# Optimization experiments

Measured on AMD Instinct MI355X. Metric: run time of the kernel, lower is better.

## Reference

```python
import jax, jax.numpy as jnp
import numpy as np

N, E, G = 8000, 128000, 4
C, NLM, NL = 64, 16, 4
NEL, NB, NH = 10, 8, 64
RMAX = 5.0
PCUT = 5.0
AVG_NEIGH = 16.0
SIGMA = 1.0
LBOX = 6.0
KR = 3
T = 2
LMAP = jnp.array([0, 1, 1, 1, 2, 2, 2, 2, 2, 3, 3, 3, 3, 3, 3, 3])


def _nvec():
    r = np.arange(-KR, KR + 1)
    n = np.stack(np.meshgrid(r, r, r, indexing='ij'), -1).reshape(-1, 3)
    n = n[np.any(n != 0, axis=1)]  # [342,3], k=0 excluded
    return jnp.asarray(n, jnp.float32)


def sph_harm(u):
    # component-normalized real spherical harmonics up to l=3, unit input u [E,3]
    x, y, z = u[:, 0], u[:, 1], u[:, 2]
    one = jnp.ones_like(x)
    c3, c5, c15 = 3.0 ** 0.5, 5.0 ** 0.5, 15.0 ** 0.5
    Y = [one,
         c3 * x, c3 * y, c3 * z,
         c15 * x * y, c15 * y * z, 0.5 * c5 * (3 * z * z - 1.0), c15 * x * z, 0.5 * c15 * (x * x - y * y),
         (35.0 / 8.0) ** 0.5 * y * (3 * x * x - y * y), 105.0 ** 0.5 * x * y * z,
         (21.0 / 8.0) ** 0.5 * y * (5 * z * z - 1.0), 0.5 * 7.0 ** 0.5 * z * (5 * z * z - 3.0),
         (21.0 / 8.0) ** 0.5 * x * (5 * z * z - 1.0), 0.5 * 105.0 ** 0.5 * z * (x * x - y * y),
         (35.0 / 8.0) ** 0.5 * x * (x * x - 3 * y * y)]
    return jnp.stack(Y, -1)  # [E,16]


def radial_basis(r):
    # Bessel basis * polynomial cutoff (MACE RadialEmbeddingBlock)
    u = r / RMAX
    n = jnp.arange(1, NB + 1, dtype=jnp.float32)
    bes = (2.0 / RMAX) ** 0.5 * jnp.sin(n[None, :] * jnp.pi * u[:, None]) / (r[:, None] + 1e-9)
    p = PCUT
    fc = 1.0 - 0.5 * (p + 1) * (p + 2) * u ** p + p * (p + 2) * u ** (p + 1) - 0.5 * p * (p + 1) * u ** (p + 2)
    fc = fc * (u < 1.0)
    return bes * fc[:, None]  # [E,8]


def setup_inputs() -> dict:
    key = jax.random.key(0)
    ks = jax.random.split(key, 24)

    def p(k, shape, fan_in):
        return jax.random.normal(k, shape, jnp.float32) / (fan_in ** 0.5)

    elem = jax.random.randint(ks[0], (N,), 0, NEL)
    inp = {
        'node_attrs': jax.nn.one_hot(elem, NEL, dtype=jnp.float32),
        'positions': jax.random.uniform(ks[1], (N, 3), jnp.float32) * LBOX,
        'shifts': jnp.zeros((E, 3), jnp.float32),
        'density_coefficients': jax.random.normal(ks[2], (N, 1), jnp.float32) * 0.1,
        'cell': jnp.tile(jnp.eye(3, dtype=jnp.float32) * LBOX, (G, 1, 1)),
        'rcell': jnp.tile(jnp.eye(3, dtype=jnp.float32) / LBOX, (G, 1, 1)),
        'volume': jnp.full((G,), LBOX ** 3, jnp.float32),
        'edge_index': jax.random.randint(ks[3], (2, E), 0, N),
        'batch': jnp.repeat(jnp.arange(G), N // G),
        'emb_W': p(ks[4], (NEL, C), NEL),
        'q_coef': p(ks[5], (T, C), 1),
        'rad_W1': p(ks[6], (T, NB, NH), NB),
        'rad_W2': p(ks[7], (T, NH, NH), NH),
        'rad_W3': p(ks[8], (T, NH, NH), NH),
        'rad_W4': p(ks[9], (T, NH, C * NL), NH),
        'lin_up': p(ks[10], (T, NL, C, C), C),
        'lin_out': p(ks[11], (T, NL, C, C), C),
        'W_sc': p(ks[12], (T, NEL, C, C), C),
        'Wp': p(ks[13], (T, 3, C, C), C),
        'W_read0': p(ks[14], (C,), C),
        'Wread1_a': p(ks[15], (C, 16), C),
        'Wread1_b': p(ks[16], (16,), 16),
        'Wq_read': p(ks[17], (T, C), C),
        'atomic_E': jax.random.normal(ks[18], (NEL,), jnp.float32),
    }
    return inp


def reference(node_attrs, positions, shifts, density_coefficients, cell, rcell, volume,
              edge_index, batch, emb_W, q_coef, rad_W1, rad_W2, rad_W3, rad_W4,
              lin_up, lin_out, W_sc, Wp, W_read0, Wread1_a, Wread1_b, Wq_read, atomic_E):
    sender, receiver = edge_index[0], edge_index[1]
    vec = positions[receiver] - positions[sender] + shifts
    r = jnp.linalg.norm(vec, axis=-1)
    Y = sph_harm(vec / (r[:, None] + 1e-9))      # [E,16]
    ef = radial_basis(r)                          # [E,8]

    q = density_coefficients                      # [N,1], max_l=0 multipoles
    feats = jnp.zeros((N, C, NLM), jnp.float32).at[:, :, 0].set(node_attrs @ emb_W)
    e0 = jax.ops.segment_sum(node_attrs @ atomic_E, batch, G)
    energies = [e0]

    for t in range(T):
        # charge-coefficient injection (charge_coefs_linears)
        feats = feats.at[:, :, 0].add(q * q_coef[t][None, :])
        # per-l linear up
        h = jnp.einsum('ncl,lcd->ndl', feats, lin_up[t][LMAP])
        # radial MLP -> per-edge, per-channel, per-l tensor-product weights
        w = jax.nn.silu(ef @ rad_W1[t])
        w = jax.nn.silu(w @ rad_W2[t])
        w = jax.nn.silu(w @ rad_W3[t])
        w = (w @ rad_W4[t]).reshape(E, C, NL)[:, :, LMAP]   # [E,C,16]
        # depthwise equivariant TP message: gather -> contract -> modulate
        hj = h[sender]                                       # [E,C,16]
        s_e = jnp.einsum('ecl,el->ec', hj, Y)                # edge invariant
        m = w * (Y[:, None, :] * s_e[:, :, None])            # [E,C,16]
        A = jax.ops.segment_sum(m, receiver, N) / AVG_NEIGH  # scatter-reduce
        A = jnp.einsum('ncl,lcd->ndl', A, lin_out[t][LMAP])
        # element-dependent residual (self-connection)
        wn = jnp.einsum('nk,kcd->ncd', node_attrs, W_sc[t])
        sc = jnp.einsum('ncd,ncl->ndl', wn, feats)
        # product block: correlation-3 symmetric-contraction surrogate
        s1 = jnp.sum(A * A, axis=2)                           # [N,C]
        out = (jnp.einsum('ncl,cd->ndl', A, Wp[t, 0])
               + jnp.einsum('ncl,cd->ndl', A * s1[:, :, None], Wp[t, 1])
               + jnp.einsum('ncl,cd->ndl', A * (s1 * s1)[:, :, None], Wp[t, 2]))
        feats = out + sc
        # readout
        if t == T - 1:
            node_e = jax.nn.silu(feats[:, :, 0] @ Wread1_a) @ Wread1_b
        else:
            node_e = feats[:, :, 0] @ W_read0
        node_e = node_e + q[:, 0] * (feats[:, :, 0] @ Wq_read[t])
        energies.append(jax.ops.segment_sum(node_e, batch, G))

    # k-space (Ewald-like) electrostatics with Gaussian-smeared charges
    nv = _nvec()                                              # [K,3]
    kvec = 2.0 * jnp.pi * jnp.einsum('kj,gji->gki', nv, rcell)  # [G,K,3]
    k2 = jnp.sum(kvec * kvec, -1)                             # [G,K]
    phase = jnp.einsum('ni,nki->nk', positions, kvec[batch])  # [N,K]
    Sr = jax.ops.segment_sum(q * jnp.cos(phase), batch, G)
    Si = jax.ops.segment_sum(q * jnp.sin(phase), batch, G)
    filt = jnp.exp(-0.5 * SIGMA * SIGMA * k2) / k2
    Ees = (2.0 * jnp.pi / volume) * jnp.sum(filt * (Sr * Sr + Si * Si), axis=1)

    total_energy = jnp.sum(jnp.stack(energies, -1), -1) + Ees
    total_charge = jax.ops.segment_sum(q[:, 0], batch, G)
    dipole = jax.ops.segment_sum(q * positions, batch, G)
    return total_energy, total_charge, dipole
```

## Files before the change

### kernel.cpp

```cpp
#include <hip/hip_runtime.h>
#include <hip/hip_bf16.h>

constexpr int N    = 8000;
constexpr int E    = 128000;
constexpr int G    = 4;
constexpr int NEL  = 10;
constexpr int NGR  = N / G;
constexpr int NC   = N * 64;
constexpr int NK   = 342;
constexpr float RMAX = 5.0f;
constexpr int XS = 68;
constexpr int HS = 72;
constexpr int WT_T = 25088;

typedef __bf16 bf16x8 __attribute__((ext_vector_type(8)));
typedef float  f32x4v __attribute__((ext_vector_type(4)));
typedef unsigned short u16x8 __attribute__((ext_vector_type(8)));

__device__ __forceinline__ int lmap_rt(int l) { return (l >= 1) + (l >= 4) + (l >= 9); }
__device__ __forceinline__ float silu(float x) { return x / (1.f + __expf(-x)); }
__device__ __forceinline__ float bf2f(unsigned short u) { return __uint_as_float(((unsigned)u) << 16); }
__device__ __forceinline__ unsigned short f2bf(float f) {
    __hip_bfloat16 h = __float2bfloat16(f);
    return *(unsigned short*)&h;
}

__device__ __forceinline__ void gemm64(const float* X, const float* W,
                                       int tr, int tc, float4 acc[4])
{
    #pragma unroll 2
    for (int k0 = 0; k0 < 64; k0 += 4) {
        float4 xq[4];
        #pragma unroll
        for (int j = 0; j < 4; ++j) xq[j] = *(const float4*)&X[((tr << 2) + j) * XS + k0];
        #pragma unroll
        for (int i = 0; i < 4; ++i) {
            const float4 w = *(const float4*)&W[((k0 + i) << 6) + (tc << 2)];
            #pragma unroll
            for (int j = 0; j < 4; ++j) {
                const float x = ((const float*)&xq[j])[i];
                acc[j].x += x * w.x; acc[j].y += x * w.y; acc[j].z += x * w.z; acc[j].w += x * w.w;
            }
        }
    }
}

__device__ __forceinline__ void mfma_stage(const unsigned short* hsrc, const unsigned short* wt,
                                           int m0, int lane, f32x4v acc[4], bool k8only)
{
    const int quad = lane >> 4;
    const int idx  = lane & 15;
    bf16x8 bz;
    #pragma unroll
    for (int i = 0; i < 8; ++i) bz[i] = (__bf16)0.f;
    bf16x8 a0 = bz, a1 = bz;
    const int mrow = m0 + idx;
    if (k8only) {
        if (quad == 0) a0 = *(const bf16x8*)&hsrc[mrow * HS];
    } else {
        a0 = *(const bf16x8*)&hsrc[mrow * HS + (quad << 3)];
        a1 = *(const bf16x8*)&hsrc[mrow * HS + 32 + (quad << 3)];
    }
    #pragma unroll
    for (int c4 = 0; c4 < 4; ++c4) {
        const int nrow = (c4 << 4) + idx;
        if (k8only) {
            bf16x8 b0 = bz;
            if (quad == 0) b0 = *(const bf16x8*)&wt[nrow * HS];
            acc[c4] = __builtin_amdgcn_mfma_f32_16x16x32_bf16(a0, b0, acc[c4], 0, 0, 0);
        } else {
            const bf16x8 b0 = *(const bf16x8*)&wt[nrow * HS + (quad << 3)];
            const bf16x8 b1 = *(const bf16x8*)&wt[nrow * HS + 32 + (quad << 3)];
            acc[c4] = __builtin_amdgcn_mfma_f32_16x16x32_bf16(a0, b0, acc[c4], 0, 0, 0);
            acc[c4] = __builtin_amdgcn_mfma_f32_16x16x32_bf16(a1, b1, acc[c4], 0, 0, 0);
        }
    }
}

__global__ __launch_bounds__(256) void k_init(const float* __restrict__ na,
    const float* __restrict__ q, const float* __restrict__ pos,
    const int* __restrict__ batch, const float* __restrict__ aE,
    int* __restrict__ elem, float* __restrict__ acc)
{
    __shared__ float s[G * 5];
    if (threadIdx.x < G * 5) s[threadIdx.x] = 0.f;
    __syncthreads();
    const int n = blockIdx.x * 256 + threadIdx.x;
    if (n < N) {
        int el = 0; float best = na[n * NEL];
        #pragma unroll
        for (int j = 1; j < NEL; ++j) { float v = na[n * NEL + j]; if (v > best) { best = v; el = j; } }
        elem[n] = el;
        const int g = batch[n];
        const float qn = q[n];
        atomicAdd(&s[g * 5 + 0], aE[el]);
        atomicAdd(&s[g * 5 + 1], qn);
        atomicAdd(&s[g * 5 + 2], qn * pos[n * 3 + 0]);
        atomicAdd(&s[g * 5 + 3], qn * pos[n * 3 + 1]);
        atomicAdd(&s[g * 5 + 4], qn * pos[n * 3 + 2]);
    }
    __syncthreads();
    if (threadIdx.x < G * 5) atomicAdd(&acc[threadIdx.x], s[threadIdx.x]);
}

__global__ __launch_bounds__(256) void k_feat0(const int* __restrict__ elem,
    const float* __restrict__ embW, float* __restrict__ F)
{
    const int i = blockIdx.x * 256 + threadIdx.x;
    if (i < NC) F[i] = embW[elem[i >> 6] * 64 + (i & 63)];
}

__global__ __launch_bounds__(256) void k_pre(const float* __restrict__ q,
    const float* __restrict__ qc, float* __restrict__ F)
{
    const int i = blockIdx.x * 256 + threadIdx.x;
    if (i < NC) F[i] += q[i >> 6] * qc[i & 63];
}

__global__ __launch_bounds__(256) void k_hist(const int* __restrict__ elem, int* __restrict__ counts)
{
    const int n = blockIdx.x * 256 + threadIdx.x;
    if (n < N) atomicAdd(&counts[elem[n]], 1);
}
__global__ void k_offs(const int* __restrict__ counts, int* __restrict__ offs)
{
    if (threadIdx.x == 0 && blockIdx.x == 0) {
        int o = 0;
        for (int j = 0; j < NEL; ++j) { offs[j] = o; o += (counts[j] + 63) & ~63; }
        offs[NEL] = o;
    }
}
__global__ __launch_bounds__(256) void k_scatter(const int* __restrict__ elem,
    const int* __restrict__ offs, int* __restrict__ cursor, int* __restrict__ perm)
{
    const int n = blockIdx.x * 256 + threadIdx.x;
    if (n < N) {
        const int el = elem[n];
        const int p = atomicAdd(&cursor[el], 1);
        perm[offs[el] + p] = n;
    }
}

__global__ __launch_bounds__(256) void k_gcnt(const int* __restrict__ ei, int* __restrict__ cnt)
{
    const int e = blockIdx.x * 256 + threadIdx.x;
    if (e < E) atomicAdd(&cnt[ei[E + e]], 1);
}
__global__ __launch_bounds__(1024) void k_goff(const int* __restrict__ cnt, int* __restrict__ roff)
{
    __shared__ int part[1024];
    const int t = threadIdx.x;
    const int base = t * 8;
    int loc[8];
    int s = 0;
    #pragma unroll
    for (int i = 0; i < 8; ++i) { loc[i] = s; s += (base + i < N) ? cnt[base + i] : 0; }
    part[t] = s;
    __syncthreads();
    for (int d = 1; d < 1024; d <<= 1) {
        const int v = (t >= d) ? part[t - d] : 0;
        __syncthreads();
        part[t] += v;
        __syncthreads();
    }
    const int excl = (t == 0) ? 0 : part[t - 1];
    #pragma unroll
    for (int i = 0; i < 8; ++i) if (base + i < N) roff[base + i] = excl + loc[i];
    if (t == 0) roff[N] = E;
}
__global__ __launch_bounds__(256) void k_gscat(const int* __restrict__ ei,
    const int* __restrict__ roff, int* __restrict__ cur, int* __restrict__ elist)
{
    const int e = blockIdx.x * 256 + threadIdx.x;
    if (e < E) {
        const int rv = ei[E + e];
        const int p = atomicAdd(&cur[rv], 1);
        elist[roff[rv] + p] = e;
    }
}

__global__ __launch_bounds__(256) void k_geom(const float* __restrict__ pos,
    const float* __restrict__ shifts, const int* __restrict__ ei,
    const int* __restrict__ elist, float4* __restrict__ geomv, int* __restrict__ spck)
{
    const int j = blockIdx.x * 256 + threadIdx.x;
    if (j >= E) return;
    const int e = elist[j];
    const int s = ei[e], rv = ei[E + e];
    const float dx = pos[rv * 3 + 0] - pos[s * 3 + 0] + shifts[e * 3 + 0];
    const float dy = pos[rv * 3 + 1] - pos[s * 3 + 1] + shifts[e * 3 + 1];
    const float dz = pos[rv * 3 + 2] - pos[s * 3 + 2] + shifts[e * 3 + 2];
    const float r = sqrtf(dx * dx + dy * dy + dz * dz);
    const float inv = 1.f / (r + 1e-9f);
    float4 g;
    g.x = dx * inv; g.y = dy * inv; g.z = dz * inv; g.w = r;
    geomv[j] = g;
    spck[j] = s;
}

__global__ __launch_bounds__(256) void k_wprep(const float* __restrict__ rW1,
    const float* __restrict__ rW2, const float* __restrict__ rW3,
    const float* __restrict__ rW4, unsigned short* __restrict__ WT)
{
    const int idx = blockIdx.x * 256 + threadIdx.x;
    if (idx >= 2 * WT_T) return;
    const int t = idx / WT_T;
    const int r = idx % WT_T;
    float v;
    if (r < 512) {
        const int n = r >> 3, k = r & 7;
        v = rW1[t * 512 + k * 64 + n];
    } else if (r < 4608) {
        const int i = r - 512, n = i >> 6, k = i & 63;
        v = rW2[t * 4096 + k * 64 + n];
    } else if (r < 8704) {
        const int i = r - 4608, n = i >> 6, k = i & 63;
        v = rW3[t * 4096 + k * 64 + n];
    } else {
        const int i = r - 8704, n = i >> 6, k = i & 63;
        v = rW4[t * 16384 + k * 256 + n];
    }
    WT[idx] = f2bf(v);
}

__global__ __launch_bounds__(256) void k_wprep2(const float* __restrict__ Wp,
    unsigned short* __restrict__ WpT)
{
    const int idx = blockIdx.x * 256 + threadIdx.x;
    if (idx >= 24576) return;
    const int tp = idx / 4096;
    const int i  = idx % 4096;
    const int d = i >> 6, c = i & 63;
    WpT[idx] = f2bf(Wp[(size_t)tp * 4096 + c * 64 + d]);
}

__global__ __launch_bounds__(256) void k_lgemm_hb(const float* __restrict__ X,
    const float* __restrict__ Wb, unsigned short* __restrict__ Hb)
{
    __shared__ float Ws[4096];
    __shared__ float Xs[64 * XS];
    const int l  = blockIdx.y;
    const int nb = blockIdx.x << 6;
    const float* W = Wb + lmap_rt(l) * 4096;
    for (int i = threadIdx.x; i < 4096; i += 256) Ws[i] = W[i];
    const float* Xp = X + (size_t)l * NC + (size_t)nb * 64;
    for (int i = threadIdx.x; i < 4096; i += 256) Xs[(i >> 6) * XS + (i & 63)] = Xp[i];
    __syncthreads();
    const int tc = threadIdx.x & 15;
    const int tr = threadIdx.x >> 4;
    float4 acc[4];
    #pragma unroll
    for (int j = 0; j < 4; ++j) acc[j] = make_float4(0.f, 0.f, 0.f, 0.f);
    gemm64(Xs, Ws, tr, tc, acc);
    #pragma unroll
    for (int j = 0; j < 4; ++j) {
        const int n = nb + (tr << 2) + j;
        ushort4 o;
        o.x = f2bf(acc[j].x); o.y = f2bf(acc[j].y); o.z = f2bf(acc[j].z); o.w = f2bf(acc[j].w);
        *(ushort4*)&Hb[(size_t)n * 1024 + (l << 6) + (tc << 2)] = o;
    }
}

__global__ __launch_bounds__(256) void k_lgemm(const float* __restrict__ X,
    const float* __restrict__ Wb, float* __restrict__ Out)
{
    __shared__ float Ws[4096];
    __shared__ float Xs[64 * XS];
    const int l  = blockIdx.y;
    const int nb = blockIdx.x << 6;
    const float* W = Wb + lmap_rt(l) * 4096;
    for (int i = threadIdx.x; i < 4096; i += 256) Ws[i] = W[i];
    const float* Xp = X + (size_t)l * NC + (size_t)nb * 64;
    for (int i = threadIdx.x; i < 4096; i += 256) Xs[(i >> 6) * XS + (i & 63)] = Xp[i];
    __syncthreads();
    const int tc = threadIdx.x & 15;
    const int tr = threadIdx.x >> 4;
    float4 acc[4];
    #pragma unroll
    for (int j = 0; j < 4; ++j) acc[j] = make_float4(0.f, 0.f, 0.f, 0.f);
    gemm64(Xs, Ws, tr, tc, acc);
    float* Op = Out + (size_t)l * NC + (size_t)nb * 64;
    #pragma unroll
    for (int j = 0; j < 4; ++j)
        *(float4*)&Op[(((tr << 2) + j) << 6) + (tc << 2)] = acc[j];
}

__global__ __launch_bounds__(256) void k_sc(const float* __restrict__ F,
    const float* __restrict__ Wsc, const int* __restrict__ perm,
    const int* __restrict__ elem, float* __restrict__ Out)
{
    __shared__ float Ws[4096];
    __shared__ float Xs[64 * XS];
    __shared__ int rows[64];
    const int l  = blockIdx.y;
    const int tb = blockIdx.x << 6;
    if (threadIdx.x < 64) rows[threadIdx.x] = perm[tb + threadIdx.x];
    __syncthreads();
    if (rows[0] < 0) return;
    const float* W = Wsc + elem[rows[0]] * 4096;
    for (int i = threadIdx.x; i < 4096; i += 256) Ws[i] = W[i];
    for (int i = threadIdx.x; i < 4096; i += 256) {
        const int rr = i >> 6, cc = i & 63;
        const int n = rows[rr];
        Xs[rr * XS + cc] = (n >= 0) ? F[(size_t)l * NC + (size_t)n * 64 + cc] : 0.f;
    }
    __syncthreads();
    const int tc = threadIdx.x & 15;
    const int tr = threadIdx.x >> 4;
    float4 acc[4];
    #pragma unroll
    for (int j = 0; j < 4; ++j) acc[j] = make_float4(0.f, 0.f, 0.f, 0.f);
    gemm64(Xs, Ws, tr, tc, acc);
    #pragma unroll
    for (int j = 0; j < 4; ++j) {
        const int n = rows[(tr << 2) + j];
        if (n >= 0) *(float4*)&Out[(size_t)l * NC + (size_t)n * 64 + (tc << 2)] = acc[j];
    }
}

__global__ __launch_bounds__(256) void k_wgemm(const float4* __restrict__ geomv,
    const unsigned short* __restrict__ WT, unsigned short* __restrict__ wout)
{
    __shared__ unsigned short hbf[64 * HS];
    __shared__ unsigned short wtb[2][64 * HS];
    __shared__ unsigned short outS[64 * HS];
    const int t = threadIdx.x;
    const int lane = t & 63;
    const int wid  = t >> 6;
    const int m0   = wid << 4;
    const int quad = lane >> 4;
    const int idx  = lane & 15;
    const int j0 = blockIdx.x << 6;
    if (t < 64) {
        const float r = geomv[j0 + t].w;
        const float u  = r * 0.2f;
        const float u2 = u * u, u5 = u2 * u2 * u;
        const float fc = 1.f - 21.f * u5 + 35.f * u5 * u - 15.f * u5 * u2;
        float pref = 0.63245553f * fc / (r + 1e-9f);
        if (u >= 1.f) pref = 0.f;
        const float piu = 3.14159265358979f * u;
        #pragma unroll
        for (int b = 0; b < 8; ++b) hbf[t * HS + b] = f2bf(__sinf((float)(b + 1) * piu) * pref);
    }
    {
        const int n = t >> 2, k = (t & 3) << 1;
        wtb[0][n * HS + k]     = WT[n * 8 + k];
        wtb[0][n * HS + k + 1] = WT[n * 8 + k + 1];
    }
    const int prow = t >> 2, pkb = (t & 3) << 4;
    u16x8 pf0, pf1;
    pf0 = *(const u16x8*)&WT[512 + prow * 64 + pkb];
    pf1 = *(const u16x8*)&WT[512 + prow * 64 + pkb + 8];
    __syncthreads();
    f32x4v acc[4];
    #pragma unroll
    for (int c = 0; c < 4; ++c) { acc[c][0] = 0.f; acc[c][1] = 0.f; acc[c][2] = 0.f; acc[c][3] = 0.f; }
    mfma_stage(hbf, wtb[0], m0, lane, acc, true);
    __syncthreads();
    #pragma unroll
    for (int c4 = 0; c4 < 4; ++c4)
        #pragma unroll
        for (int r = 0; r < 4; ++r)
            hbf[(m0 + (quad << 2) + r) * HS + (c4 << 4) + idx] = f2bf(silu(acc[c4][r]));
    *(u16x8*)&wtb[1][prow * HS + pkb]     = pf0;
    *(u16x8*)&wtb[1][prow * HS + pkb + 8] = pf1;
    pf0 = *(const u16x8*)&WT[4608 + prow * 64 + pkb];
    pf1 = *(const u16x8*)&WT[4608 + prow * 64 + pkb + 8];
    __syncthreads();
    #pragma unroll
    for (int c = 0; c < 4; ++c) { acc[c][0] = 0.f; acc[c][1] = 0.f; acc[c][2] = 0.f; acc[c][3] = 0.f; }
    mfma_stage(hbf, wtb[1], m0, lane, acc, false);
    __syncthreads();
    #pragma unroll
    for (int c4 = 0; c4 < 4; ++c4)
        #pragma unroll
        for (int r = 0; r < 4; ++r)
            hbf[(m0 + (quad << 2) + r) * HS + (c4 << 4) + idx] = f2bf(silu(acc[c4][r]));
    *(u16x8*)&wtb[0][prow * HS + pkb]     = pf0;
    *(u16x8*)&wtb[0][prow * HS + pkb + 8] = pf1;
    pf0 = *(const u16x8*)&WT[8704 + prow * 64 + pkb];
    pf1 = *(const u16x8*)&WT[8704 + prow * 64 + pkb + 8];
    __syncthreads();
    #pragma unroll
    for (int c = 0; c < 4; ++c) { acc[c][0] = 0.f; acc[c][1] = 0.f; acc[c][2] = 0.f; acc[c][3] = 0.f; }
    mfma_stage(hbf, wtb[0], m0, lane, acc, false);
    __syncthreads();
    #pragma unroll
    for (int c4 = 0; c4 < 4; ++c4)
        #pragma unroll
        for (int r = 0; r < 4; ++r)
            hbf[(m0 + (quad << 2) + r) * HS + (c4 << 4) + idx] = f2bf(silu(acc[c4][r]));
    *(u16x8*)&wtb[1][prow * HS + pkb]     = pf0;
    *(u16x8*)&wtb[1][prow * HS + pkb + 8] = pf1;
    pf0 = *(const u16x8*)&WT[8704 + 4096 + prow * 64 + pkb];
    pf1 = *(const u16x8*)&WT[8704 + 4096 + prow * 64 + pkb + 8];
    __syncthreads();
    int cur = 1;
    for (int c = 0; c < 4; ++c) {
        #pragma unroll
        for (int cc = 0; cc < 4; ++cc) { acc[cc][0] = 0.f; acc[cc][1] = 0.f; acc[cc][2] = 0.f; acc[cc][3] = 0.f; }
        mfma_stage(hbf, wtb[cur], m0, lane, acc, false);
        __syncthreads();
        #pragma unroll
        for (int c4 = 0; c4 < 4; ++c4)
            #pragma unroll
            for (int r = 0; r < 4; ++r)
                outS[(m0 + (quad << 2) + r) * HS + (c4 << 4) + idx] = f2bf(acc[c4][r]);
        if (c < 3) {
            *(u16x8*)&wtb[1 - cur][prow * HS + pkb]     = pf0;
            *(u16x8*)&wtb[1 - cur][prow * HS + pkb + 8] = pf1;
            if (c < 2) {
                pf0 = *(const u16x8*)&WT[8704 + (c + 2) * 4096 + prow * 64 + pkb];
                pf1 = *(const u16x8*)&WT[8704 + (c + 2) * 4096 + prow * 64 + pkb + 8];
            }
        }
        __syncthreads();
        *(u16x8*)&wout[(size_t)(j0 + prow) * 256 + (c << 6) + pkb]     = *(const u16x8*)&outS[prow * HS + pkb];
        *(u16x8*)&wout[(size_t)(j0 + prow) * 256 + (c << 6) + pkb + 8] = *(const u16x8*)&outS[prow * HS + pkb + 8];
        cur ^= 1;
    }
}

__global__ __launch_bounds__(256) void k_agg(const float4* __restrict__ geomv,
    const int* __restrict__ spck,
    const unsigned short* __restrict__ Hb, const unsigned short* __restrict__ wb,
    const int* __restrict__ roff, float* __restrict__ A)
{
    const int lane = threadIdx.x & 63;
    const int n = (blockIdx.x << 2) + (threadIdx.x >> 6);
    const int ja = roff[n], jb2 = roff[n + 1];
    float acc[16];
    #pragma unroll
    for (int l = 0; l < 16; ++l) acc[l] = 0.f;
    constexpr int LM[16] = {0,1,1,1,2,2,2,2,2,3,3,3,3,3,3,3};
    float4 g0, g1;
    ushort4 w0, w1;
    int s1_ = 0;
    unsigned short hv0[16];
    if (ja < jb2) {
        g0 = geomv[ja];
        const int s0 = spck[ja];
        w0 = *(const ushort4*)&wb[(size_t)ja * 256 + (lane << 2)];
        #pragma unroll
        for (int l = 0; l < 16; ++l) hv0[l] = Hb[(size_t)s0 * 1024 + (l << 6) + lane];
    }
    if (ja + 1 < jb2) {
        g1 = geomv[ja + 1];
        s1_ = spck[ja + 1];
        w1 = *(const ushort4*)&wb[(size_t)(ja + 1) * 256 + (lane << 2)];
    }
    for (int j = ja; j < jb2; ++j) {
        const float4 gc = g0;
        const ushort4 wc = w0;
        float hc[16];
        #pragma unroll
        for (int l = 0; l < 16; ++l) hc[l] = bf2f(hv0[l]);
        if (j + 1 < jb2) {
            g0 = g1; w0 = w1;
            const int sN = s1_;
            #pragma unroll
            for (int l = 0; l < 16; ++l) hv0[l] = Hb[(size_t)sN * 1024 + (l << 6) + lane];
            if (j + 2 < jb2) {
                g1 = geomv[j + 2];
                s1_ = spck[j + 2];
                w1 = *(const ushort4*)&wb[(size_t)(j + 2) * 256 + (lane << 2)];
            }
        }
        if (gc.w >= RMAX) continue;
        const float x = gc.x, y = gc.y, z = gc.z;
        const float xx = x * x, yy = y * y, zz = z * z;
        float Y[16];
        Y[0] = 1.f;
        Y[1] = 1.7320508f * x;  Y[2] = 1.7320508f * y;  Y[3] = 1.7320508f * z;
        Y[4] = 3.8729833f * x * y;  Y[5] = 3.8729833f * y * z;
        Y[6] = 0.5f * 2.2360680f * (3.f * zz - 1.f);
        Y[7] = 3.8729833f * x * z;  Y[8] = 0.5f * 3.8729833f * (xx - yy);
        Y[9]  = 2.0916500f * y * (3.f * xx - yy);
        Y[10] = 10.2469508f * x * y * z;
        Y[11] = 1.6201852f * y * (5.f * zz - 1.f);
        Y[12] = 0.5f * 2.6457513f * z * (5.f * zz - 3.f);
        Y[13] = 1.6201852f * x * (5.f * zz - 1.f);
        Y[14] = 0.5f * 10.2469508f * z * (xx - yy);
        Y[15] = 2.0916500f * x * (xx - 3.f * yy);
        float se = 0.f;
        #pragma unroll
        for (int l = 0; l < 16; ++l) se += hc[l] * Y[l];
        se *= 0.0625f;
        const float wl[4] = { bf2f(wc.x) * se, bf2f(wc.y) * se, bf2f(wc.z) * se, bf2f(wc.w) * se };
        #pragma unroll
        for (int l = 0; l < 16; ++l) acc[l] += wl[LM[l]] * Y[l];
    }
    float* Ap = A + (size_t)n * 64 + lane;
    #pragma unroll
    for (int l = 0; l < 16; ++l) Ap[(size_t)l * NC] = acc[l];
}

__global__ __launch_bounds__(256) void k_s1(const float* __restrict__ H, float* __restrict__ s1)
{
    const int i = blockIdx.x * 256 + threadIdx.x;
    if (i < NC) {
        float s = 0.f;
        #pragma unroll
        for (int l = 0; l < 16; ++l) { const float a = H[(size_t)l * NC + i]; s += a * a; }
        s1[i] = s;
    }
}

__global__ __launch_bounds__(256) void k_out(const float* __restrict__ Ap,
    const float* __restrict__ s1, const unsigned short* __restrict__ WpT,
    const float* __restrict__ sc, float* __restrict__ F)
{
    __shared__ unsigned short Xb[64 * HS];
    __shared__ unsigned short Wt[64 * HS];
    const int l  = blockIdx.y;
    const int nb = blockIdx.x << 6;
    const int t  = threadIdx.x;
    const int lane = t & 63;
    const int m0   = (t >> 6) << 4;
    const int quad = lane >> 4;
    const int idx  = lane & 15;
    const int prow = t >> 2, pkb = (t & 3) << 4;
    const float* Xp = Ap + (size_t)l * NC + (size_t)nb * 64;
    float av[16], sv[16];
    #pragma unroll
    for (int k = 0; k < 16; ++k) {
        const int i = t + (k << 8);
        av[k] = Xp[i];
        sv[k] = s1[nb * 64 + i];
    }
    f32x4v acc[4];
    #pragma unroll
    for (int c = 0; c < 4; ++c) { acc[c][0] = 0.f; acc[c][1] = 0.f; acc[c][2] = 0.f; acc[c][3] = 0.f; }
    for (int p = 0; p < 3; ++p) {
        #pragma unroll
        for (int k = 0; k < 16; ++k) {
            const int i = t + (k << 8);
            Xb[(i >> 6) * HS + (i & 63)] = f2bf(av[k]);
            av[k] *= sv[k];
        }
        *(u16x8*)&Wt[prow * HS + pkb]     = *(const u16x8*)&WpT[p * 4096 + prow * 64 + pkb];
        *(u16x8*)&Wt[prow * HS + pkb + 8] = *(const u16x8*)&WpT[p * 4096 + prow * 64 + pkb + 8];
        __syncthreads();
        mfma_stage(Xb, Wt, m0, lane, acc, false);
        __syncthreads();
    }
    #pragma unroll
    for (int c4 = 0; c4 < 4; ++c4) {
        #pragma unroll
        for (int r = 0; r < 4; ++r) {
            const int row = m0 + (quad << 2) + r;
            const int col = (c4 << 4) + idx;
            const size_t id = (size_t)l * NC + (size_t)(nb + row) * 64 + col;
            F[id] = acc[c4][r] + sc[id];
        }
    }
}

__global__ __launch_bounds__(256) void k_read(const float* __restrict__ F,
    const float* __restrict__ q, const int* __restrict__ batch,
    const float* __restrict__ Wr0, const float* __restrict__ Wa,
    const float* __restrict__ Wb, const float* __restrict__ Wq,
    float* __restrict__ acc, int last)
{
    __shared__ float sred[G];
    if (threadIdx.x < G) sred[threadIdx.x] = 0.f;
    __syncthreads();
    const int n = blockIdx.x * 256 + threadIdx.x;
    if (n < N) {
        float a16[16];
        #pragma unroll
        for (int j = 0; j < 16; ++j) a16[j] = 0.f;
        float ar = 0.f, aq = 0.f;
        const float* f = F + (size_t)n * 64;
        for (int c = 0; c < 64; ++c) {
            const float fv = f[c];
            aq += fv * Wq[c];
            if (last) {
                #pragma unroll
                for (int j = 0; j < 16; ++j) a16[j] += fv * Wa[c * 16 + j];
            } else ar += fv * Wr0[c];
        }
        float en;
        if (last) {
            en = 0.f;
            #pragma unroll
            for (int j = 0; j < 16; ++j) en += silu(a16[j]) * Wb[j];
        } else en = ar;
        en += q[n] * aq;
        atomicAdd(&sred[batch[n]], en);
    }
    __syncthreads();
    if (threadIdx.x < G) atomicAdd(&acc[threadIdx.x * 5], sred[threadIdx.x]);
}

__global__ __launch_bounds__(256) void k_kvec(const float* __restrict__ rcell,
    float* __restrict__ kvec, float* __restrict__ k2)
{
    const int idx = blockIdx.x * 256 + threadIdx.x;
    if (idx >= G * NK) return;
    const int g = idx / NK, k = idx % NK;
    const int kk = k + (k >= 171 ? 1 : 0);
    const int a = kk / 49 - 3, b = (kk / 7) % 7 - 3, c = kk % 7 - 3;
    const float* rc = rcell + g * 9;
    float s = 0.f;
    #pragma unroll
    for (int i = 0; i < 3; ++i) {
        const float kv = 6.283185307f * ((float)a * rc[0 + i] + (float)b * rc[3 + i] + (float)c * rc[6 + i]);
        kvec[idx * 3 + i] = kv;
        s += kv * kv;
    }
    k2[idx] = s;
}

__global__ __launch_bounds__(256) void k_phase(const float* __restrict__ pos,
    const float* __restrict__ q, const float* __restrict__ kvec,
    float* __restrict__ Sr, float* __restrict__ Si)
{
    __shared__ float kvs[38 * 3];
    __shared__ float srs[38], sis[38];
    const int g = blockIdx.z, kc = blockIdx.x, ncb = blockIdx.y;
    const int kbase = kc * 38;
    if (threadIdx.x < 38 * 3) kvs[threadIdx.x] = kvec[((size_t)g * NK + kbase) * 3 + threadIdx.x];
    if (threadIdx.x < 38) { srs[threadIdx.x] = 0.f; sis[threadIdx.x] = 0.f; }
    __syncthreads();
    const int t = threadIdx.x;
    float px = 0.f, py = 0.f, pz = 0.f, qn = 0.f;
    if (t < 250) {
        const int n = g * NGR + ncb * 250 + t;
        px = pos[n * 3]; py = pos[n * 3 + 1]; pz = pos[n * 3 + 2]; qn = q[n];
    }
    const int lane = t & 63;
    for (int j = 0; j < 38; ++j) {
        const float ph = px * kvs[j * 3] + py * kvs[j * 3 + 1] + pz * kvs[j * 3 + 2];
        float sv, cv;
        __sincosf(ph, &sv, &cv);
        float vr = qn * cv, vi = qn * sv;
        #pragma unroll
        for (int o = 32; o > 0; o >>= 1) { vr += __shfl_down(vr, o, 64); vi += __shfl_down(vi, o, 64); }
        if (lane == 0) { atomicAdd(&srs[j], vr); atomicAdd(&sis[j], vi); }
    }
    __syncthreads();
    if (t < 38) {
        atomicAdd(&Sr[g * NK + kbase + t], srs[t]);
        atomicAdd(&Si[g * NK + kbase + t], sis[t]);
    }
}

__global__ __launch_bounds__(512) void k_final(const float* __restrict__ k2,
    const float* __restrict__ Sr, const float* __restrict__ Si,
    const float* __restrict__ vol, const float* __restrict__ acc,
    float* __restrict__ out)
{
    __shared__ float red[512];
    const int g = blockIdx.x, t = threadIdx.x;
    float v = 0.f;
    if (t < NK) {
        const float kk = k2[g * NK + t];
        const float sr = Sr[g * NK + t], si = Si[g * NK + t];
        v = __expf(-0.5f * kk) * (sr * sr + si * si) / kk;
    }
    red[t] = v;
    __syncthreads();
    for (int s2 = 256; s2 > 0; s2 >>= 1) {
        if (t < s2) red[t] += red[t + s2];
        __syncthreads();
    }
    if (t == 0) {
        const float Ees = 6.283185307f / vol[g] * red[0];
        out[g]     = acc[g * 5 + 0] + Ees;
        out[4 + g] = acc[g * 5 + 1];
        out[8 + g * 3 + 0] = acc[g * 5 + 2];
        out[8 + g * 3 + 1] = acc[g * 5 + 3];
        out[8 + g * 3 + 2] = acc[g * 5 + 4];
    }
}

extern "C" void kernel_launch(void* const* d_in, const int* in_sizes, int n_in,
                              void* d_out, int out_size, void* d_ws, size_t ws_size,
                              hipStream_t stream)
{
    const float* na    = (const float*)d_in[0];
    const float* pos   = (const float*)d_in[1];
    const float* shif  = (const float*)d_in[2];
    const float* q     = (const float*)d_in[3];
    const float* rcell = (const float*)d_in[5];
    const float* vol   = (const float*)d_in[6];
    const int*   ei    = (const int*)d_in[7];
    const int*   batch = (const int*)d_in[8];
    const float* embW  = (const float*)d_in[9];
    const float* qcoef = (const float*)d_in[10];
    const float* rW1   = (const float*)d_in[11];
    const float* rW2   = (const float*)d_in[12];
    const float* rW3   = (const float*)d_in[13];
    const float* rW4   = (const float*)d_in[14];
    const float* lup   = (const float*)d_in[15];
    const float* lout  = (const float*)d_in[16];
    const float* Wsc   = (const float*)d_in[17];
    const float* Wp    = (const float*)d_in[18];
    const float* Wr0   = (const float*)d_in[19];
    const float* Wa    = (const float*)d_in[20];
    const float* Wb    = (const float*)d_in[21];
    const float* Wq    = (const float*)d_in[22];
    const float* aE    = (const float*)d_in[23];
    float* out = (float*)d_out;

    float* wsf  = (float*)d_ws;
    float* F    = wsf;
    float* A    = F + 8192000;
    float* R    = A + 8192000;
    float* H2   = R;
    unsigned short* Hb = (unsigned short*)R;
    unsigned short* wb = (unsigned short*)(R + 4096000);
    float* s1   = R + 20480000;
    float* kvec = s1 + 512000;
    float* k2   = kvec + 4104;
    float* Sr   = k2 + 1368;
    float* Si   = Sr + 1368;
    float* acc  = Si + 1368;
    int*   elem = (int*)(acc + 32);
    int*   perm = elem + 8000;
    int*   counts = perm + 8640;
    int*   cursor = counts + 16;
    int*   offs   = cursor + 16;
    int*   roff   = offs + 16;
    int*   cnt    = roff + 8001;
    int*   cur    = cnt + 8000;
    int*   elist  = cur + 8000;
    unsigned short* WTb = (unsigned short*)(((uintptr_t)(elist + E) + 31) & ~(uintptr_t)31);
    unsigned short* WpT = WTb + 2 * WT_T;
    float4* geomv = (float4*)(WpT + 24576);
    int*    spck  = (int*)(geomv + E);

    hipMemsetAsync(F, 0, 8192000 * sizeof(float), stream);
    hipMemsetAsync(Sr, 0, (1368 * 2 + 32) * sizeof(float), stream);
    hipMemsetAsync(perm, 0xFF, 8640 * sizeof(int), stream);
    hipMemsetAsync(counts, 0, 32 * sizeof(int), stream);
    hipMemsetAsync(cnt, 0, 16000 * sizeof(int), stream);

    k_init<<<32, 256, 0, stream>>>(na, q, pos, batch, aE, elem, acc);
    k_feat0<<<2000, 256, 0, stream>>>(elem, embW, F);
    k_hist<<<32, 256, 0, stream>>>(elem, counts);
    k_offs<<<1, 64, 0, stream>>>(counts, offs);
    k_scatter<<<32, 256, 0, stream>>>(elem, offs, cursor, perm);
    k_gcnt<<<500, 256, 0, stream>>>(ei, cnt);
    k_goff<<<1, 1024, 0, stream>>>(cnt, roff);
    k_gscat<<<500, 256, 0, stream>>>(ei, roff, cur, elist);
    k_geom<<<500, 256, 0, stream>>>(pos, shif, ei, elist, geomv, spck);
    k_wprep<<<196, 256, 0, stream>>>(rW1, rW2, rW3, rW4, WTb);
    k_wprep2<<<96, 256, 0, stream>>>(Wp, WpT);
    k_kvec<<<6, 256, 0, stream>>>(rcell, kvec, k2);
    k_phase<<<dim3(9, 8, G), 256, 0, stream>>>(pos, q, kvec, Sr, Si);

    for (int t = 0; t < 2; ++t) {
        k_pre<<<2000, 256, 0, stream>>>(q, qcoef + t * 64, F);
        k_lgemm_hb<<<dim3(125, 16), 256, 0, stream>>>(F, lup + t * 4 * 4096, Hb);
        k_wgemm<<<2000, 256, 0, stream>>>(geomv, WTb + t * WT_T, wb);
        k_agg<<<2000, 256, 0, stream>>>(geomv, spck, Hb, wb, roff, A);
        k_lgemm<<<dim3(125, 16), 256, 0, stream>>>(A, lout + t * 4 * 4096, H2);
        k_s1<<<2000, 256, 0, stream>>>(H2, s1);
        k_sc<<<dim3(135, 16), 256, 0, stream>>>(F, Wsc + t * NEL * 4096, perm, elem, A);
        k_out<<<dim3(125, 16), 256, 0, stream>>>(H2, s1, WpT + t * 12288, A, F);
        k_read<<<32, 256, 0, stream>>>(F, q, batch, Wr0, Wa, Wb, Wq + t * 64, acc, t == 1);
    }
    k_final<<<G, 512, 0, stream>>>(k2, Sr, Si, vol, acc, out);
}
```

Measured before the change: 649.5 us.

## Move per-l channel GEMMs to bf16 MFMA and deepen agg edge prefetch

The three 64x64 fp32 FMA GEMM kernels (lgemm_hb, lgemm, sc) now convert inputs to bf16 in shared memory and use the existing MFMA stage. Their weights are pre-transposed into bf16 by a new prep kernel. The aggregation kernel's edge loop is restructured with a three-deep clamped prefetch of geometry, weights and source indices. This cuts FMA issue and shared-memory traffic, but lowers GEMM input precision to bf16 and adds a prep launch.

New measurement: 564.4 us. -13.1%, faster.

```diff
diff --git a/kernel.cpp b/kernel.cpp
--- a/kernel.cpp
+++ b/kernel.cpp
@@ -9,7 +9,6 @@
 constexpr int NC   = N * 64;
 constexpr int NK   = 342;
 constexpr float RMAX = 5.0f;
-constexpr int XS = 68;
 constexpr int HS = 72;
 constexpr int WT_T = 25088;
 
@@ -23,26 +22,6 @@
 __device__ __forceinline__ unsigned short f2bf(float f) {
     __hip_bfloat16 h = __float2bfloat16(f);
     return *(unsigned short*)&h;
-}
-
-__device__ __forceinline__ void gemm64(const float* X, const float* W,
-                                       int tr, int tc, float4 acc[4])
-{
-    #pragma unroll 2
-    for (int k0 = 0; k0 < 64; k0 += 4) {
-        float4 xq[4];
-        #pragma unroll
-        for (int j = 0; j < 4; ++j) xq[j] = *(const float4*)&X[((tr << 2) + j) * XS + k0];
-        #pragma unroll
-        for (int i = 0; i < 4; ++i) {
-            const float4 w = *(const float4*)&W[((k0 + i) << 6) + (tc << 2)];
-            #pragma unroll
-            for (int j = 0; j < 4; ++j) {
-                const float x = ((const float*)&xq[j])[i];
-                acc[j].x += x * w.x; acc[j].y += x * w.y; acc[j].z += x * w.z; acc[j].w += x * w.w;
-            }
-        }
-    }
 }
 
 __device__ __forceinline__ void mfma_stage(const unsigned short* hsrc, const unsigned short* wt,
@@ -234,87 +213,142 @@
     WpT[idx] = f2bf(Wp[(size_t)tp * 4096 + c * 64 + d]);
 }
 
+__global__ __launch_bounds__(256) void k_wprep3(const float* __restrict__ lup,
+    const float* __restrict__ lout, const float* __restrict__ Wsc,
+    unsigned short* __restrict__ WlupT, unsigned short* __restrict__ WloutT,
+    unsigned short* __restrict__ WscT)
+{
+    const int idx = blockIdx.x * 256 + threadIdx.x;
+    if (idx < 32768) {
+        const int i = idx & 4095, d = i >> 6, c = i & 63;
+        WlupT[idx] = f2bf(lup[(idx >> 12) * 4096 + c * 64 + d]);
+    } else if (idx < 65536) {
+        const int r = idx - 32768;
+        const int i = r & 4095, d = i >> 6, c = i & 63;
+        WloutT[r] = f2bf(lout[(r >> 12) * 4096 + c * 64 + d]);
+    } else if (idx < 147456) {
+        const int r = idx - 65536;
+        const int i = r & 4095, d = i >> 6, c = i & 63;
+        WscT[r] = f2bf(Wsc[(r >> 12) * 4096 + c * 64 + d]);
+    }
+}
+
 __global__ __launch_bounds__(256) void k_lgemm_hb(const float* __restrict__ X,
-    const float* __restrict__ Wb, unsigned short* __restrict__ Hb)
-{
-    __shared__ float Ws[4096];
-    __shared__ float Xs[64 * XS];
+    const unsigned short* __restrict__ WT, unsigned short* __restrict__ Hb)
+{
+    __shared__ unsigned short Xb[64 * HS];
+    __shared__ unsigned short Wt[64 * HS];
     const int l  = blockIdx.y;
     const int nb = blockIdx.x << 6;
-    const float* W = Wb + lmap_rt(l) * 4096;
-    for (int i = threadIdx.x; i < 4096; i += 256) Ws[i] = W[i];
+    const int t  = threadIdx.x;
+    const int lane = t & 63;
+    const int m0   = (t >> 6) << 4;
+    const int quad = lane >> 4;
+    const int idx  = lane & 15;
+    const int prow = t >> 2, pkb = (t & 3) << 4;
     const float* Xp = X + (size_t)l * NC + (size_t)nb * 64;
-    for (int i = threadIdx.x; i < 4096; i += 256) Xs[(i >> 6) * XS + (i & 63)] = Xp[i];
-    __syncthreads();
-    const int tc = threadIdx.x & 15;
-    const int tr = threadIdx.x >> 4;
-    float4 acc[4];
-    #pragma unroll
-    for (int j = 0; j < 4; ++j) acc[j] = make_float4(0.f, 0.f, 0.f, 0.f);
-    gemm64(Xs, Ws, tr, tc, acc);
-    #pragma unroll
-    for (int j = 0; j < 4; ++j) {
-        const int n = nb + (tr << 2) + j;
-        ushort4 o;
-        o.x = f2bf(acc[j].x); o.y = f2bf(acc[j].y); o.z = f2bf(acc[j].z); o.w = f2bf(acc[j].w);
-        *(ushort4*)&Hb[(size_t)n * 1024 + (l << 6) + (tc << 2)] = o;
+    #pragma unroll
+    for (int k = 0; k < 16; ++k) {
+        const int i = t + (k << 8);
+        Xb[(i >> 6) * HS + (i & 63)] = f2bf(Xp[i]);
+    }
+    const unsigned short* W = WT + lmap_rt(l) * 4096;
+    *(u16x8*)&Wt[prow * HS + pkb]     = *(const u16x8*)&W[prow * 64 + pkb];
+    *(u16x8*)&Wt[prow * HS + pkb + 8] = *(const u16x8*)&W[prow * 64 + pkb + 8];
+    __syncthreads();
+    f32x4v acc[4];
+    #pragma unroll
+    for (int c = 0; c < 4; ++c) { acc[c][0] = 0.f; acc[c][1] = 0.f; acc[c][2] = 0.f; acc[c][3] = 0.f; }
+    mfma_stage(Xb, Wt, m0, lane, acc, false);
+    #pragma unroll
+    for (int c4 = 0; c4 < 4; ++c4) {
+        #pragma unroll
+        for (int r = 0; r < 4; ++r) {
+            const int n = nb + m0 + (quad << 2) + r;
+            const int col = (c4 << 4) + idx;
+            Hb[(size_t)n * 1024 + (l << 6) + col] = f2bf(acc[c4][r]);
+        }
     }
 }
 
 __global__ __launch_bounds__(256) void k_lgemm(const float* __restrict__ X,
-    const float* __restrict__ Wb, float* __restrict__ Out)
-{
-    __shared__ float Ws[4096];
-    __shared__ float Xs[64 * XS];
+    const unsigned short* __restrict__ WT, float* __restrict__ Out)
+{
+    __shared__ unsigned short Xb[64 * HS];
+    __shared__ unsigned short Wt[64 * HS];
     const int l  = blockIdx.y;
     const int nb = blockIdx.x << 6;
-    const float* W = Wb + lmap_rt(l) * 4096;
-    for (int i = threadIdx.x; i < 4096; i += 256) Ws[i] = W[i];
+    const int t  = threadIdx.x;
+    const int lane = t & 63;
+    const int m0   = (t >> 6) << 4;
+    const int quad = lane >> 4;
+    const int idx  = lane & 15;
+    const int prow = t >> 2, pkb = (t & 3) << 4;
     const float* Xp = X + (size_t)l * NC + (size_t)nb * 64;
-    for (int i = threadIdx.x; i < 4096; i += 256) Xs[(i >> 6) * XS + (i & 63)] = Xp[i];
-    __syncthreads();
-    const int tc = threadIdx.x & 15;
-    const int tr = threadIdx.x >> 4;
-    float4 acc[4];
-    #pragma unroll
-    for (int j = 0; j < 4; ++j) acc[j] = make_float4(0.f, 0.f, 0.f, 0.f);
-    gemm64(Xs, Ws, tr, tc, acc);
+    #pragma unroll
+    for (int k = 0; k < 16; ++k) {
+        const int i = t + (k << 8);
+        Xb[(i >> 6) * HS + (i & 63)] = f2bf(Xp[i]);
+    }
+    const unsigned short* W = WT + lmap_rt(l) * 4096;
+    *(u16x8*)&Wt[prow * HS + pkb]     = *(const u16x8*)&W[prow * 64 + pkb];
+    *(u16x8*)&Wt[prow * HS + pkb + 8] = *(const u16x8*)&W[prow * 64 + pkb + 8];
+    __syncthreads();
+    f32x4v acc[4];
+    #pragma unroll
+    for (int c = 0; c < 4; ++c) { acc[c][0] = 0.f; acc[c][1] = 0.f; acc[c][2] = 0.f; acc[c][3] = 0.f; }
+    mfma_stage(Xb, Wt, m0, lane, acc, false);
     float* Op = Out + (size_t)l * NC + (size_t)nb * 64;
     #pragma unroll
-    for (int j = 0; j < 4; ++j)
-        *(float4*)&Op[(((tr << 2) + j) << 6) + (tc << 2)] = acc[j];
+    for (int c4 = 0; c4 < 4; ++c4) {
+        #pragma unroll
+        for (int r = 0; r < 4; ++r) {
+            const int row = m0 + (quad << 2) + r;
+            Op[(row << 6) + (c4 << 4) + idx] = acc[c4][r];
+        }
+    }
 }
 
 __global__ __launch_bounds__(256) void k_sc(const float* __restrict__ F,
-    const float* __restrict__ Wsc, const int* __restrict__ perm,
+    const unsigned short* __restrict__ WscT, const int* __restrict__ perm,
     const int* __restrict__ elem, float* __restrict__ Out)
 {
-    __shared__ float Ws[4096];
-    __shared__ float Xs[64 * XS];
+    __shared__ unsigned short Xb[64 * HS];
+    __shared__ unsigned short Wt[64 * HS];
     __shared__ int rows[64];
     const int l  = blockIdx.y;
     const int tb = blockIdx.x << 6;
-    if (threadIdx.x < 64) rows[threadIdx.x] = perm[tb + threadIdx.x];
+    const int t  = threadIdx.x;
+    if (t < 64) rows[t] = perm[tb + t];
     __syncthreads();
     if (rows[0] < 0) return;
-    const float* W = Wsc + elem[rows[0]] * 4096;
-    for (int i = threadIdx.x; i < 4096; i += 256) Ws[i] = W[i];
-    for (int i = threadIdx.x; i < 4096; i += 256) {
+    const int lane = t & 63;
+    const int m0   = (t >> 6) << 4;
+    const int quad = lane >> 4;
+    const int idx  = lane & 15;
+    const int prow = t >> 2, pkb = (t & 3) << 4;
+    const unsigned short* W = WscT + elem[rows[0]] * 4096;
+    *(u16x8*)&Wt[prow * HS + pkb]     = *(const u16x8*)&W[prow * 64 + pkb];
+    *(u16x8*)&Wt[prow * HS + pkb + 8] = *(const u16x8*)&W[prow * 64 + pkb + 8];
+    #pragma unroll
+    for (int k = 0; k < 16; ++k) {
+        const int i = t + (k << 8);
         const int rr = i >> 6, cc = i & 63;
         const int n = rows[rr];
-        Xs[rr * XS + cc] = (n >= 0) ? F[(size_t)l * NC + (size_t)n * 64 + cc] : 0.f;
-    }
-    __syncthreads();
-    const int tc = threadIdx.x & 15;
-    const int tr = threadIdx.x >> 4;
-    float4 acc[4];
-    #pragma unroll
-    for (int j = 0; j < 4; ++j) acc[j] = make_float4(0.f, 0.f, 0.f, 0.f);
-    gemm64(Xs, Ws, tr, tc, acc);
-    #pragma unroll
-    for (int j = 0; j < 4; ++j) {
-        const int n = rows[(tr << 2) + j];
-        if (n >= 0) *(float4*)&Out[(size_t)l * NC + (size_t)n * 64 + (tc << 2)] = acc[j];
+        Xb[rr * HS + cc] = (n >= 0) ? f2bf(F[(size_t)l * NC + (size_t)n * 64 + cc]) : (unsigned short)0;
+    }
+    __syncthreads();
+    f32x4v acc[4];
+    #pragma unroll
+    for (int c = 0; c < 4; ++c) { acc[c][0] = 0.f; acc[c][1] = 0.f; acc[c][2] = 0.f; acc[c][3] = 0.f; }
+    mfma_stage(Xb, Wt, m0, lane, acc, false);
+    #pragma unroll
+    for (int c4 = 0; c4 < 4; ++c4) {
+        #pragma unroll
+        for (int r = 0; r < 4; ++r) {
+            const int n = rows[m0 + (quad << 2) + r];
+            if (n >= 0) Out[(size_t)l * NC + (size_t)n * 64 + (c4 << 4) + idx] = acc[c4][r];
+        }
     }
 }
 
@@ -429,70 +463,68 @@
     const int lane = threadIdx.x & 63;
     const int n = (blockIdx.x << 2) + (threadIdx.x >> 6);
     const int ja = roff[n], jb2 = roff[n + 1];
-    float acc[16];
-    #pragma unroll
-    for (int l = 0; l < 16; ++l) acc[l] = 0.f;
+    float accv[16];
+    #pragma unroll
+    for (int l = 0; l < 16; ++l) accv[l] = 0.f;
     constexpr int LM[16] = {0,1,1,1,2,2,2,2,2,3,3,3,3,3,3,3};
-    float4 g0, g1;
-    ushort4 w0, w1;
-    int s1_ = 0;
-    unsigned short hv0[16];
     if (ja < jb2) {
-        g0 = geomv[ja];
-        const int s0 = spck[ja];
-        w0 = *(const ushort4*)&wb[(size_t)ja * 256 + (lane << 2)];
-        #pragma unroll
-        for (int l = 0; l < 16; ++l) hv0[l] = Hb[(size_t)s0 * 1024 + (l << 6) + lane];
-    }
-    if (ja + 1 < jb2) {
-        g1 = geomv[ja + 1];
-        s1_ = spck[ja + 1];
-        w1 = *(const ushort4*)&wb[(size_t)(ja + 1) * 256 + (lane << 2)];
-    }
-    for (int j = ja; j < jb2; ++j) {
-        const float4 gc = g0;
-        const ushort4 wc = w0;
-        float hc[16];
-        #pragma unroll
-        for (int l = 0; l < 16; ++l) hc[l] = bf2f(hv0[l]);
-        if (j + 1 < jb2) {
-            g0 = g1; w0 = w1;
-            const int sN = s1_;
+        const int jlast = jb2 - 1;
+        int j1c = ja + 1 < jlast ? ja + 1 : jlast;
+        int j2c = ja + 2 < jlast ? ja + 2 : jlast;
+        float4 g0 = geomv[ja],  g1 = geomv[j1c],  g2 = geomv[j2c];
+        ushort4 w0 = *(const ushort4*)&wb[(size_t)ja * 256 + (lane << 2)];
+        ushort4 w1 = *(const ushort4*)&wb[(size_t)j1c * 256 + (lane << 2)];
+        ushort4 w2 = *(const ushort4*)&wb[(size_t)j2c * 256 + (lane << 2)];
+        int sB = spck[j1c], sC = spck[j2c];
+        unsigned short hv[16];
+        {
+            const int s0 = spck[ja];
             #pragma unroll
-            for (int l = 0; l < 16; ++l) hv0[l] = Hb[(size_t)sN * 1024 + (l << 6) + lane];
-            if (j + 2 < jb2) {
-                g1 = geomv[j + 2];
-                s1_ = spck[j + 2];
-                w1 = *(const ushort4*)&wb[(size_t)(j + 2) * 256 + (lane << 2)];
+            for (int l = 0; l < 16; ++l) hv[l] = Hb[(size_t)s0 * 1024 + (l << 6) + lane];
+        }
+        for (int j = ja; j < jb2; ++j) {
+            const float4 gc = g0;
+            const ushort4 wc = w0;
+            float hc[16];
+            #pragma unroll
+            for (int l = 0; l < 16; ++l) hc[l] = bf2f(hv[l]);
+            g0 = g1; g1 = g2; w0 = w1; w1 = w2;
+            const int sA = sB; sB = sC;
+            #pragma unroll
+            for (int l = 0; l < 16; ++l) hv[l] = Hb[(size_t)sA * 1024 + (l << 6) + lane];
+            const int j3 = j + 3 < jlast ? j + 3 : jlast;
+            g2 = geomv[j3];
+            w2 = *(const ushort4*)&wb[(size_t)j3 * 256 + (lane << 2)];
+            sC = spck[j3];
+            if (gc.w < RMAX) {
+                const float x = gc.x, y = gc.y, z = gc.z;
+                const float xx = x * x, yy = y * y, zz = z * z;
+                float Y[16];
+                Y[0] = 1.f;
+                Y[1] = 1.7320508f * x;  Y[2] = 1.7320508f * y;  Y[3] = 1.7320508f * z;
+                Y[4] = 3.8729833f * x * y;  Y[5] = 3.8729833f * y * z;
+                Y[6] = 0.5f * 2.2360680f * (3.f * zz - 1.f);
+                Y[7] = 3.8729833f * x * z;  Y[8] = 0.5f * 3.8729833f * (xx - yy);
+                Y[9]  = 2.0916500f * y * (3.f * xx - yy);
+                Y[10] = 10.2469508f * x * y * z;
+                Y[11] = 1.6201852f * y * (5.f * zz - 1.f);
+                Y[12] = 0.5f * 2.6457513f * z * (5.f * zz - 3.f);
+                Y[13] = 1.6201852f * x * (5.f * zz - 1.f);
+                Y[14] = 0.5f * 10.2469508f * z * (xx - yy);
+                Y[15] = 2.0916500f * x * (xx - 3.f * yy);
+                float se = 0.f;
+                #pragma unroll
+                for (int l = 0; l < 16; ++l) se += hc[l] * Y[l];
+                se *= 0.0625f;
+                const float wl[4] = { bf2f(wc.x) * se, bf2f(wc.y) * se, bf2f(wc.z) * se, bf2f(wc.w) * se };
+                #pragma unroll
+                for (int l = 0; l < 16; ++l) accv[l] += wl[LM[l]] * Y[l];
             }
         }
-        if (gc.w >= RMAX) continue;
-        const float x = gc.x, y = gc.y, z = gc.z;
-        const float xx = x * x, yy = y * y, zz = z * z;
-        float Y[16];
-        Y[0] = 1.f;
-        Y[1] = 1.7320508f * x;  Y[2] = 1.7320508f * y;  Y[3] = 1.7320508f * z;
-        Y[4] = 3.8729833f * x * y;  Y[5] = 3.8729833f * y * z;
-        Y[6] = 0.5f * 2.2360680f * (3.f * zz - 1.f);
-        Y[7] = 3.8729833f * x * z;  Y[8] = 0.5f * 3.8729833f * (xx - yy);
-        Y[9]  = 2.0916500f * y * (3.f * xx - yy);
-        Y[10] = 10.2469508f * x * y * z;
-        Y[11] = 1.6201852f * y * (5.f * zz - 1.f);
-        Y[12] = 0.5f * 2.6457513f * z * (5.f * zz - 3.f);
-        Y[13] = 1.6201852f * x * (5.f * zz - 1.f);
-        Y[14] = 0.5f * 10.2469508f * z * (xx - yy);
-        Y[15] = 2.0916500f * x * (xx - 3.f * yy);
-        float se = 0.f;
-        #pragma unroll
-        for (int l = 0; l < 16; ++l) se += hc[l] * Y[l];
-        se *= 0.0625f;
-        const float wl[4] = { bf2f(wc.x) * se, bf2f(wc.y) * se, bf2f(wc.z) * se, bf2f(wc.w) * se };
-        #pragma unroll
-        for (int l = 0; l < 16; ++l) acc[l] += wl[LM[l]] * Y[l];
     }
     float* Ap = A + (size_t)n * 64 + lane;
     #pragma unroll
-    for (int l = 0; l < 16; ++l) Ap[(size_t)l * NC] = acc[l];
+    for (int l = 0; l < 16; ++l) Ap[(size_t)l * NC] = accv[l];
 }
 
 __global__ __launch_bounds__(256) void k_s1(const float* __restrict__ H, float* __restrict__ s1)
@@ -730,6 +762,9 @@
     unsigned short* WpT = WTb + 2 * WT_T;
     float4* geomv = (float4*)(WpT + 24576);
     int*    spck  = (int*)(geomv + E);
+    unsigned short* WlupT  = (unsigned short*)(spck + E);
+    unsigned short* WloutT = WlupT + 32768;
+    unsigned short* WscT   = WloutT + 32768;
 
     hipMemsetAsync(F, 0, 8192000 * sizeof(float), stream);
     hipMemsetAsync(Sr, 0, (1368 * 2 + 32) * sizeof(float), stream);
@@ -748,17 +783,18 @@
     k_geom<<<500, 256, 0, stream>>>(pos, shif, ei, elist, geomv, spck);
     k_wprep<<<196, 256, 0, stream>>>(rW1, rW2, rW3, rW4, WTb);
     k_wprep2<<<96, 256, 0, stream>>>(Wp, WpT);
+    k_wprep3<<<576, 256, 0, stream>>>(lup, lout, Wsc, WlupT, WloutT, WscT);
     k_kvec<<<6, 256, 0, stream>>>(rcell, kvec, k2);
     k_phase<<<dim3(9, 8, G), 256, 0, stream>>>(pos, q, kvec, Sr, Si);
 
     for (int t = 0; t < 2; ++t) {
         k_pre<<<2000, 256, 0, stream>>>(q, qcoef + t * 64, F);
-        k_lgemm_hb<<<dim3(125, 16), 256, 0, stream>>>(F, lup + t * 4 * 4096, Hb);
+        k_lgemm_hb<<<dim3(125, 16), 256, 0, stream>>>(F, WlupT + t * 16384, Hb);
         k_wgemm<<<2000, 256, 0, stream>>>(geomv, WTb + t * WT_T, wb);
         k_agg<<<2000, 256, 0, stream>>>(geomv, spck, Hb, wb, roff, A);
-        k_lgemm<<<dim3(125, 16), 256, 0, stream>>>(A, lout + t * 4 * 4096, H2);
+        k_lgemm<<<dim3(125, 16), 256, 0, stream>>>(A, WloutT + t * 16384, H2);
         k_s1<<<2000, 256, 0, stream>>>(H2, s1);
-        k_sc<<<dim3(135, 16), 256, 0, stream>>>(F, Wsc + t * NEL * 4096, perm, elem, A);
+        k_sc<<<dim3(135, 16), 256, 0, stream>>>(F, WscT + t * 40960, perm, elem, A);
         k_out<<<dim3(125, 16), 256, 0, stream>>>(H2, s1, WpT + t * 12288, A, F);
         k_read<<<32, 256, 0, stream>>>(F, q, batch, Wr0, Wa, Wb, Wq + t * 64, acc, t == 1);
     }
```
